# Kernel tuning notes

Hardware: AMD Instinct MI355X
Metric: run time of the kernel (lower is better)

Reference implementation:

```python
import jax, jax.numpy as jnp
import numpy as np

N = 50000      # num_labels (nodes)
HID = 64       # hidden_dim
HEADS = 4
CH = 16        # hidden_dim // 4 per head
R = 4          # relations
E = 200000     # edges per relation
DEPTH = 2
SLOPE = 0.2    # GATv2 leaky_relu negative slope
EPS = 1e-5     # LayerNorm eps


def layer_norm(x, g, b):
    mu = jnp.mean(x, axis=-1, keepdims=True)
    var = jnp.mean((x - mu) ** 2, axis=-1, keepdims=True)
    return (x - mu) / jnp.sqrt(var + EPS) * g + b


def setup_inputs() -> dict:
    key = jax.random.key(0)
    ks = jax.random.split(key, 8)
    # edges with src != dst (PyG remove_self_loops is then a no-op)
    src = jax.random.randint(ks[0], (R, E), 0, N, dtype=jnp.int32)
    off = jax.random.randint(ks[1], (R, E), 1, N, dtype=jnp.int32)
    dst = ((src + off) % N).astype(jnp.int32)
    edge_index = jnp.stack([src, dst], axis=1)  # [R, 2, E]
    s = 1.0 / np.sqrt(HID)
    return {
        "label_embeddings": jax.random.normal(ks[2], (N, HID), jnp.float32) * 0.5,
        "entry_w": jax.random.normal(ks[3], (HID, HID), jnp.float32) * s,
        "entry_b": jnp.zeros((HID,), jnp.float32),
        "entry_ln_g": jnp.ones((HID,), jnp.float32),
        "entry_ln_b": jnp.zeros((HID,), jnp.float32),
        "conv_wl": jax.random.normal(ks[4], (DEPTH, R, HID, HEADS * CH), jnp.float32) * s,
        "conv_wr": jax.random.normal(ks[5], (DEPTH, R, HID, HEADS * CH), jnp.float32) * s,
        "conv_att": jax.random.normal(ks[6], (DEPTH, R, HEADS, CH), jnp.float32) * (1.0 / np.sqrt(CH)),
        "conv_bias": jnp.zeros((DEPTH, R, HEADS * CH), jnp.float32),
        "norm_g": jnp.ones((HID,), jnp.float32),
        "norm_b": jnp.zeros((HID,), jnp.float32),
        "edge_index": edge_index,
    }


def _gatv2_layer(x, wl, wr, att, bias, src, dst):
    """One GATv2Conv over one relation. x:[N,HID]; returns [N, HEADS*CH]."""
    xl = (x @ wl).reshape(N, HEADS, CH)  # source transform
    xr = (x @ wr).reshape(N, HEADS, CH)  # target transform
    m = xl[src] + xr[dst]                          # [E+N, HEADS, CH]
    e = jnp.einsum('ehc,hc->eh', jax.nn.leaky_relu(m, SLOPE), att)  # [E+N, HEADS]
    # segment softmax over incoming edges of each dst node
    emax = jax.ops.segment_max(e, dst, num_segments=N)  # [N, HEADS]
    a = jnp.exp(e - emax[dst])
    denom = jax.ops.segment_sum(a, dst, num_segments=N)
    alpha = a / denom[dst]                          # every node has a self-loop -> denom > 0
    msg = xl[src] * alpha[..., None]                # [E+N, HEADS, CH]
    out = jax.ops.segment_sum(msg, dst, num_segments=N).reshape(N, HEADS * CH)
    return out + bias


def reference(label_embeddings, entry_w, entry_b, entry_ln_g, entry_ln_b,
              conv_wl, conv_wr, conv_att, conv_bias, norm_g, norm_b, edge_index):
    x = jax.nn.gelu(layer_norm(label_embeddings @ entry_w + entry_b, entry_ln_g, entry_ln_b),
                    approximate=False)
    loop = jnp.arange(N, dtype=edge_index.dtype)
    for layer in range(DEPTH):
        outs = []
        for r in range(R):
            src = jnp.concatenate([edge_index[r, 0], loop])  # add self-loops (PyG default)
            dst = jnp.concatenate([edge_index[r, 1], loop])
            outs.append(_gatv2_layer(x, conv_wl[layer, r], conv_wr[layer, r],
                                     conv_att[layer, r], conv_bias[layer, r], src, dst))
        x = sum(outs) / R                              # HeteroConv aggr='mean'
        x = layer_norm(jax.nn.gelu(x, approximate=False), norm_g, norm_b)  # dropout = identity (eval)
    return x
```

## Files before the change

kernel.cpp:

```cpp
#include <hip/hip_runtime.h>
#include <hip/hip_bf16.h>

#define NN 50000
#define RR 4
#define EE 200000

typedef __hip_bfloat16 bf16;
typedef __attribute__((ext_vector_type(8))) short short8;
typedef __attribute__((ext_vector_type(4))) float float4v;
typedef __attribute__((ext_vector_type(2))) float float2v;

__device__ __forceinline__ unsigned short f2bu(float v) {
    bf16 h = __float2bfloat16(v);
    return *(unsigned short*)&h;
}
__device__ __forceinline__ float ldf(const void* p, int i, int isbf) {
    return isbf ? __bfloat162float(((const bf16*)p)[i]) : ((const float*)p)[i];
}
__device__ __forceinline__ int dtype_isbf(const void* lg) {
    return ((const unsigned*)lg)[0] == 0x3F803F80u;
}
__device__ __forceinline__ float gelu_exact(float x) {
    return 0.5f * x * (1.0f + erff(x * 0.70710678118654752f));
}
__device__ __forceinline__ float2v bp2(unsigned u) {
    float2v f;
    f.x = __uint_as_float(u << 16);
    f.y = __uint_as_float(u & 0xffff0000u);
    return f;
}
__device__ __forceinline__ float2v lrelu2(float2v m) {
    float2v s = m * 0.2f;
    float2v r;
    r.x = fmaxf(m.x, s.x);
    r.y = fmaxf(m.y, s.y);
    return r;
}

#define PW_ENTRY_W 0
#define PW_ENTRY_B 4096
#define PW_LN_G    4160
#define PW_LN_B    4224
#define PW_WL      4288
#define PW_ATT     69824
#define PW_BIAS    70336
#define PW_NG      70848
#define PW_NB      70912
#define PW_TOT     70976

#define WT_ELEMS (2 * RR * 128 * 64)
#define SCAN_N (RR * NN)
#define NSB 196
#define ESB 196

__global__ __launch_bounds__(1024) void cvt_k(const void* ew, const void* eb, const void* lg,
                                              const void* lb, const void* wl, const void* wr,
                                              const void* at, const void* bi, const void* ng,
                                              const void* nb,
                                              float* __restrict__ P, bf16* __restrict__ WT,
                                              int* __restrict__ cnt) {
    int i = blockIdx.x * 1024 + threadIdx.x;
    int isbf = dtype_isbf(lg);
    if (i < SCAN_N) cnt[i] = 0;
    if (i < WT_ELEMS) {
        int k = i & 63;
        int c = (i >> 6) & 127;
        int lr = i >> 13;
        float v = (c < 64) ? ldf(wl, (lr * 64 + k) * 64 + c, isbf)
                           : ldf(wr, (lr * 64 + k) * 64 + (c - 64), isbf);
        WT[i] = __float2bfloat16(v);
    }
    if (i < PW_TOT) {
        const void* src = nullptr;
        int off = 0;
        if (i < PW_ENTRY_B)      { src = ew; off = i - PW_ENTRY_W; }
        else if (i < PW_LN_G)    { src = eb; off = i - PW_ENTRY_B; }
        else if (i < PW_LN_B)    { src = lg; off = i - PW_LN_G; }
        else if (i < PW_WL)      { src = lb; off = i - PW_LN_B; }
        else if (i < PW_ATT)     { src = nullptr; }
        else if (i < PW_BIAS)    { src = at; off = i - PW_ATT; }
        else if (i < PW_NG)      { src = bi; off = i - PW_BIAS; }
        else if (i < PW_NB)      { src = ng; off = i - PW_NG; }
        else                     { src = nb; off = i - PW_NB; }
        if (src) P[i] = ldf(src, off, isbf);
    }
}

#define HIST_BLOCKS 782
#define ENTRY_BLOCKS 2500
#define ENTRY_WAVES (ENTRY_BLOCKS * 4)
__global__ __launch_bounds__(256) void scent_k(const int* __restrict__ ei,
                                               int* __restrict__ cnt,
                                               unsigned char* __restrict__ slot8,
                                               const void* __restrict__ emb,
                                               const void* __restrict__ lg,
                                               const float* __restrict__ P,
                                               bf16* __restrict__ xout) {
    int b = blockIdx.x;
    if (b < HIST_BLOCKS) {
        int base = b * 1024 + threadIdx.x;
#pragma unroll
        for (int j = 0; j < 4; j++) {
            int idx = base + j * 256;
            if (idx < RR * EE) {
                int r = idx / EE;
                int e = idx - r * EE;
                int d = ei[r * 2 * EE + EE + e];
                int p = atomicAdd(&cnt[r * NN + d], 1);
                slot8[idx] = (unsigned char)p;
            }
        }
        return;
    }
    int wv = (b - HIST_BLOCKS) * 4 + (threadIdx.x >> 6);
    int c = threadIdx.x & 63;
    int isbf = dtype_isbf(lg);
    for (int j = 0; j < 5; j++) {
        int node = wv + j * ENTRY_WAVES;
        float ev = ldf(emb, node * 64 + c, isbf);
        float acc = 0.f;
#pragma unroll 8
        for (int k = 0; k < 64; k++) {
            float xv = __shfl(ev, k, 64);
            acc += xv * P[PW_ENTRY_W + k * 64 + c];
        }
        acc += P[PW_ENTRY_B + c];
        float s = acc;
#pragma unroll
        for (int m = 1; m < 64; m <<= 1) s += __shfl_xor(s, m, 64);
        float mu = s * (1.f / 64.f);
        float d = acc - mu;
        float vs = d * d;
#pragma unroll
        for (int m = 1; m < 64; m <<= 1) vs += __shfl_xor(vs, m, 64);
        float var = vs * (1.f / 64.f);
        float y = d * rsqrtf(var + 1e-5f) * P[PW_LN_G + c] + P[PW_LN_B + c];
        xout[node * 64 + c] = __float2bfloat16(gelu_exact(y));
    }
}

__global__ __launch_bounds__(256) void scanA_k(const int* __restrict__ cnt,
                                               int* __restrict__ bsum) {
    int b = blockIdx.x, t = threadIdx.x;
    int s = 0;
#pragma unroll
    for (int j = 0; j < 4; j++) {
        int i = b * 1024 + j * 256 + t;
        if (i < SCAN_N) s += cnt[i];
    }
#pragma unroll
    for (int m = 1; m < 64; m <<= 1) s += __shfl_xor(s, m, 64);
    __shared__ int ws[4];
    if ((t & 63) == 0) ws[t >> 6] = s;
    __syncthreads();
    if (t == 0) bsum[b] = ws[0] + ws[1] + ws[2] + ws[3];
}

__global__ void scanB_k(int* __restrict__ bsum, int* __restrict__ rp) {
    int l = threadIdx.x;
    int i0 = l * 4;
    int v0 = (i0 + 0 < NSB) ? bsum[i0 + 0] : 0;
    int v1 = (i0 + 1 < NSB) ? bsum[i0 + 1] : 0;
    int v2 = (i0 + 2 < NSB) ? bsum[i0 + 2] : 0;
    int v3 = (i0 + 3 < NSB) ? bsum[i0 + 3] : 0;
    int ts = v0 + v1 + v2 + v3;
    int inc = ts;
#pragma unroll
    for (int m = 1; m < 64; m <<= 1) {
        int y = __shfl_up(inc, m, 64);
        if (l >= m) inc += y;
    }
    int run = inc - ts;
    if (i0 + 0 < NSB) { bsum[i0 + 0] = run; run += v0; }
    if (i0 + 1 < NSB) { bsum[i0 + 1] = run; run += v1; }
    if (i0 + 2 < NSB) { bsum[i0 + 2] = run; run += v2; }
    if (i0 + 3 < NSB) { bsum[i0 + 3] = run; run += v3; }
    if (l == 63) rp[SCAN_N] = inc;
}

__global__ __launch_bounds__(256) void scanC_k(const int* __restrict__ cnt,
                                               const int* __restrict__ bsum,
                                               int* __restrict__ rp) {
    int b = blockIdx.x, t = threadIdx.x;
    int i0 = b * 1024 + t * 4;
    int v0 = (i0 + 0 < SCAN_N) ? cnt[i0 + 0] : 0;
    int v1 = (i0 + 1 < SCAN_N) ? cnt[i0 + 1] : 0;
    int v2 = (i0 + 2 < SCAN_N) ? cnt[i0 + 2] : 0;
    int v3 = (i0 + 3 < SCAN_N) ? cnt[i0 + 3] : 0;
    int ts = v0 + v1 + v2 + v3;
    int lane = t & 63, w = t >> 6;
    int inc = ts;
#pragma unroll
    for (int m = 1; m < 64; m <<= 1) {
        int y = __shfl_up(inc, m, 64);
        if (lane >= m) inc += y;
    }
    __shared__ int ws[4];
    if (lane == 63) ws[w] = inc;
    __syncthreads();
    int run = bsum[b];
    for (int k = 0; k < w; k++) run += ws[k];
    run += inc - ts;
    if (i0 + 0 < SCAN_N) { rp[i0 + 0] = run; run += v0; }
    if (i0 + 1 < SCAN_N) { rp[i0 + 1] = run; run += v1; }
    if (i0 + 2 < SCAN_N) { rp[i0 + 2] = run; run += v2; }
    if (i0 + 3 < SCAN_N) { rp[i0 + 3] = run; run += v3; }
}

#define GR 80
__global__ __launch_bounds__(256) void gemm_m(const bf16* __restrict__ X,
                                              const bf16* __restrict__ WTlayer,
                                              bf16* __restrict__ xlB,
                                              bf16* __restrict__ xrB,
                                              const int* __restrict__ ei,
                                              const unsigned char* __restrict__ slot8,
                                              const int* __restrict__ rp,
                                              unsigned short* __restrict__ col,
                                              int scatBlocks) {
    int bx = blockIdx.x;
    int r = blockIdx.y;
    if (bx < scatBlocks) {
        const int* eis = ei + r * 2 * EE;
#pragma unroll
        for (int j = 0; j < 4; j++) {
            int e = bx * 1024 + j * 256 + threadIdx.x;
            if (e < EE) {
                int s = eis[e];
                int d = eis[EE + e];
                int p = slot8[r * EE + e];
                col[rp[r * NN + d] + p] = (unsigned short)s;
            }
        }
        return;
    }
    const short* Xs = (const short*)X;
    const short* WT = (const short*)(WTlayer + (size_t)r * 8192);
    bf16* xl = xlB + (size_t)r * NN * 64;
    bf16* xr = xrB + (size_t)r * NN * 64;

    __shared__ float sh[16 * 132];
    int t = threadIdx.x;
    int w = t >> 6;
    int lane = t & 63;
    int m = lane & 15, kq = lane >> 4;
    int row0 = (bx - scatBlocks) * GR;

    short8 b0[2], b1[2];
    int c0t[2];
#pragma unroll
    for (int tile = 0; tile < 2; tile++) {
        int ct = w * 2 + tile;
        int c0 = ct * 16 + m;
        c0t[tile] = c0;
        const short* bp = WT + c0 * 64 + kq * 8;
        b0[tile] = *(const short8*)bp;
        b1[tile] = *(const short8*)(bp + 32);
    }

    const short* ap = Xs + (row0 + m) * 64 + kq * 8;
    short8 a0 = *(const short8*)ap;
    short8 a1 = *(const short8*)(ap + 32);

    for (int g = 0; g < 5; g++) {
        short8 na0, na1;
        if (g < 4) {
            const short* np = ap + (g + 1) * 16 * 64;
            na0 = *(const short8*)np;
            na1 = *(const short8*)(np + 32);
        }
#pragma unroll
        for (int tile = 0; tile < 2; tile++) {
            float4v acc = {0.f, 0.f, 0.f, 0.f};
            asm volatile(
                "v_mfma_f32_16x16x32_bf16 %0, %1, %2, %0\n\t"
                "v_mfma_f32_16x16x32_bf16 %0, %3, %4, %0\n\t"
                "s_nop 7\n\t"
                "s_nop 7"
                : "+v"(acc)
                : "v"(a0), "v"(b0[tile]), "v"(a1), "v"(b1[tile]));
#pragma unroll
            for (int i = 0; i < 4; i++) sh[(kq * 4 + i) * 132 + c0t[tile]] = acc[i];
        }
        __syncthreads();
        {
            int row = t >> 4, cg = (t & 15) * 8;
            float v0 = sh[row * 132 + cg + 0], v1 = sh[row * 132 + cg + 1];
            float v2 = sh[row * 132 + cg + 2], v3 = sh[row * 132 + cg + 3];
            float v4 = sh[row * 132 + cg + 4], v5 = sh[row * 132 + cg + 5];
            float v6 = sh[row * 132 + cg + 6], v7 = sh[row * 132 + cg + 7];
            uint4 u;
            u.x = ((unsigned)f2bu(v1) << 16) | f2bu(v0);
            u.y = ((unsigned)f2bu(v3) << 16) | f2bu(v2);
            u.z = ((unsigned)f2bu(v5) << 16) | f2bu(v4);
            u.w = ((unsigned)f2bu(v7) << 16) | f2bu(v6);
            size_t grow = row0 + g * 16 + row;
            if (cg < 64) *(uint4*)&xl[grow * 64 + cg] = u;
            else         *(uint4*)&xr[grow * 64 + (cg - 64)] = u;
        }
        __syncthreads();
        a0 = na0; a1 = na1;
    }
}

__device__ __forceinline__ void edge_accum(uint4 u0, uint4 u1, bool act,
                                           const float2v at2[8], const float2v xr2[8],
                                           float2v A2[8], float& D) {
    float2v x2[8];
    x2[0] = bp2(u0.x); x2[1] = bp2(u0.y); x2[2] = bp2(u0.z); x2[3] = bp2(u0.w);
    x2[4] = bp2(u1.x); x2[5] = bp2(u1.y); x2[6] = bp2(u1.z); x2[7] = bp2(u1.w);
    float2v t2 = (float2v){0.f, 0.f};
#pragma unroll
    for (int i = 0; i < 8; i++)
        t2 = t2 + lrelu2(x2[i] + xr2[i]) * at2[i];
    float tt = t2.x + t2.y;
    float p = act ? exp2f(tt) : 0.f;
    D += p;
    float2v p2 = (float2v){p, p};
#pragma unroll
    for (int i = 0; i < 8; i++) A2[i] = A2[i] + p2 * x2[i];
}

__global__ __launch_bounds__(256) void aggfin_k(const bf16* __restrict__ xlB,
                                                const bf16* __restrict__ xrB,
                                                const float* __restrict__ attL,
                                                const float* __restrict__ biasL,
                                                const int* __restrict__ rp,
                                                const unsigned short* __restrict__ col,
                                                const float* __restrict__ P,
                                                const void* __restrict__ lg,
                                                void* __restrict__ outp,
                                                int finalOut) {
    __shared__ float shRes[RR][4][68];
    int t = threadIdx.x;
    int r = t >> 6;
    int lane = t & 63;
    int nodeBase = blockIdx.x * 4;
    int nn = lane >> 4, es = (lane >> 2) & 3, h = lane & 3;
    int node = nodeBase + nn;

    const unsigned* xl = (const unsigned*)(xlB + (size_t)r * NN * 64);
    const unsigned* xr = (const unsigned*)(xrB + (size_t)r * NN * 64);
    const float* att = attL + r * 64;
    const float* bias = biasL + r * 64;

    int idx = r * NN + node;
    int base = rp[idx];
    int cn = rp[idx + 1] - base;
    const uint4* qr = (const uint4*)(xr + (size_t)node * 32 + h * 8);
    uint4 r0 = qr[0], r1 = qr[1];

    const unsigned short* bucket = col + base;
    int c0raw = (es > 0) ? (int)bucket[es - 1] : node;
    int c1raw = (int)bucket[es + 3];

    unsigned s0 = (unsigned)c0raw < (unsigned)NN ? (unsigned)c0raw : (unsigned)(NN - 1);
    unsigned s1 = (unsigned)c1raw < (unsigned)NN ? (unsigned)c1raw : (unsigned)(NN - 1);
    const uint4* q0 = (const uint4*)(xl + (size_t)s0 * 32 + h * 8);
    uint4 u0 = q0[0], u1 = q0[1];
    const uint4* q1 = (const uint4*)(xl + (size_t)s1 * 32 + h * 8);
    uint4 w0 = q1[0], w1 = q1[1];

    float2v at2[8], xr2[8];
    {
        const float4* apv = (const float4*)(att + h * 16);
#pragma unroll
        for (int i = 0; i < 4; i++) {
            float4 a = apv[i];
            at2[2 * i].x = a.x * 1.44269504f; at2[2 * i].y = a.y * 1.44269504f;
            at2[2 * i + 1].x = a.z * 1.44269504f; at2[2 * i + 1].y = a.w * 1.44269504f;
        }
        xr2[0] = bp2(r0.x); xr2[1] = bp2(r0.y); xr2[2] = bp2(r0.z); xr2[3] = bp2(r0.w);
        xr2[4] = bp2(r1.x); xr2[5] = bp2(r1.y); xr2[6] = bp2(r1.z); xr2[7] = bp2(r1.w);
    }
    int total = cn + 1;
    int kmax = total;
    kmax = max(kmax, __shfl_xor(kmax, 16, 64));
    kmax = max(kmax, __shfl_xor(kmax, 32, 64));

    float2v A2[8];
#pragma unroll
    for (int i = 0; i < 8; i++) A2[i] = (float2v){0.f, 0.f};
    float D = 0.f;

    edge_accum(u0, u1, es < total, at2, xr2, A2, D);
    edge_accum(w0, w1, es + 4 < total, at2, xr2, A2, D);

    for (int k = es + 8; k < kmax; k += 4) {
        bool act = k < total;
        int sr = act ? (int)bucket[k - 1] : node;
        const uint4* q = (const uint4*)(xl + (size_t)sr * 32 + h * 8);
        uint4 t0 = q[0], t1 = q[1];
        edge_accum(t0, t1, act, at2, xr2, A2, D);
    }

    D += __shfl_xor(D, 4, 64);
    D += __shfl_xor(D, 8, 64);
#pragma unroll
    for (int i = 0; i < 8; i++) {
        A2[i].x += __shfl_xor(A2[i].x, 4, 64);
        A2[i].x += __shfl_xor(A2[i].x, 8, 64);
        A2[i].y += __shfl_xor(A2[i].y, 4, 64);
        A2[i].y += __shfl_xor(A2[i].y, 8, 64);
    }
    if (es == 0) {
        float inv = __builtin_amdgcn_rcpf(D);
        const float4* bp = (const float4*)(bias + h * 16);
        float* dst = &shRes[r][nn][h * 16];
#pragma unroll
        for (int i = 0; i < 4; i++) {
            float4 b = bp[i];
            dst[4 * i + 0] = A2[2 * i].x * inv + b.x;
            dst[4 * i + 1] = A2[2 * i].y * inv + b.y;
            dst[4 * i + 2] = A2[2 * i + 1].x * inv + b.z;
            dst[4 * i + 3] = A2[2 * i + 1].y * inv + b.w;
        }
    }
    __syncthreads();
    int wn = t >> 6, c = t & 63;
    float v = shRes[0][wn][c] + shRes[1][wn][c] + shRes[2][wn][c] + shRes[3][wn][c];
    v = gelu_exact(v * 0.25f);
    float s = v;
#pragma unroll
    for (int m = 1; m < 64; m <<= 1) s += __shfl_xor(s, m, 64);
    float mu = s * (1.f / 64.f);
    float d = v - mu;
    float vs = d * d;
#pragma unroll
    for (int m = 1; m < 64; m <<= 1) vs += __shfl_xor(vs, m, 64);
    float var = vs * (1.f / 64.f);
    float y = d * rsqrtf(var + 1e-5f) * P[PW_NG + c] + P[PW_NB + c];
    size_t o = (size_t)(nodeBase + wn) * 64 + c;
    if (!finalOut) {
        ((bf16*)outp)[o] = __float2bfloat16(y);
    } else {
        if (dtype_isbf(lg)) ((bf16*)outp)[o] = __float2bfloat16(y);
        else                ((float*)outp)[o] = y;
    }
}

extern "C" void kernel_launch(void* const* d_in, const int* in_sizes, int n_in,
                              void* d_out, int out_size, void* d_ws, size_t ws_size,
                              hipStream_t stream) {
    const void* emb = d_in[0];
    const void* lg  = d_in[3];
    const int*  ei  = (const int*)d_in[11];

    const size_t BUF = (size_t)NN * 64;

    bf16* X   = (bf16*)d_ws;
    bf16* XL  = X + BUF;
    bf16* XR  = XL + RR * BUF;
    bf16* WT  = XR + RR * BUF;
    float* P  = (float*)(WT + WT_ELEMS);
    int* cnt  = (int*)(P + PW_TOT);
    int* rp   = cnt + SCAN_N;
    int* bsum = rp + SCAN_N + 1;
    unsigned short* col = (unsigned short*)(bsum + 256);
    unsigned char* slot8 = (unsigned char*)(col + RR * EE + 64);

    int cvtN = SCAN_N;
    cvt_k<<<(cvtN + 1023) / 1024, 1024, 0, stream>>>(d_in[1], d_in[2], d_in[3], d_in[4],
                                                     d_in[5], d_in[6], d_in[7], d_in[8],
                                                     d_in[9], d_in[10], P, WT, cnt);

    scent_k<<<HIST_BLOCKS + ENTRY_BLOCKS, 256, 0, stream>>>(ei, cnt, slot8, emb, lg, P, X);

    scanA_k<<<NSB, 256, 0, stream>>>(cnt, bsum);
    scanB_k<<<1, 64, 0, stream>>>(bsum, rp);
    scanC_k<<<NSB, 256, 0, stream>>>(cnt, bsum, rp);

    int gemmBlocks = 625;
    int nodeBlocks = NN / 4;

    for (int l = 0; l < 2; l++) {
        int sb = (l == 0) ? ESB : 0;
        gemm_m<<<dim3(sb + gemmBlocks, RR), 256, 0, stream>>>(
            X, WT + (size_t)l * RR * 8192, XL, XR, ei, slot8, rp, col, sb);
        aggfin_k<<<nodeBlocks, 256, 0, stream>>>(
            XL, XR, P + PW_ATT + (size_t)l * RR * 64, P + PW_BIAS + (size_t)l * RR * 64,
            rp, col, P, lg, (l == 0) ? (void*)X : d_out, l);
    }
}
```

Baseline: 323.6 us.

## Fold weight conversion into histogram kernel, overlap partial scan with first GEMM

```diff
diff --git a/kernel.cpp b/kernel.cpp
--- a/kernel.cpp
+++ b/kernel.cpp
@@ -51,54 +51,29 @@
 #define WT_ELEMS (2 * RR * 128 * 64)
 #define SCAN_N (RR * NN)
 #define NSB 196
-#define ESB 196
-
-__global__ __launch_bounds__(1024) void cvt_k(const void* ew, const void* eb, const void* lg,
-                                              const void* lb, const void* wl, const void* wr,
-                                              const void* at, const void* bi, const void* ng,
-                                              const void* nb,
-                                              float* __restrict__ P, bf16* __restrict__ WT,
-                                              int* __restrict__ cnt) {
-    int i = blockIdx.x * 1024 + threadIdx.x;
-    int isbf = dtype_isbf(lg);
-    if (i < SCAN_N) cnt[i] = 0;
-    if (i < WT_ELEMS) {
-        int k = i & 63;
-        int c = (i >> 6) & 127;
-        int lr = i >> 13;
-        float v = (c < 64) ? ldf(wl, (lr * 64 + k) * 64 + c, isbf)
-                           : ldf(wr, (lr * 64 + k) * 64 + (c - 64), isbf);
-        WT[i] = __float2bfloat16(v);
-    }
-    if (i < PW_TOT) {
-        const void* src = nullptr;
-        int off = 0;
-        if (i < PW_ENTRY_B)      { src = ew; off = i - PW_ENTRY_W; }
-        else if (i < PW_LN_G)    { src = eb; off = i - PW_ENTRY_B; }
-        else if (i < PW_LN_B)    { src = lg; off = i - PW_LN_G; }
-        else if (i < PW_WL)      { src = lb; off = i - PW_LN_B; }
-        else if (i < PW_ATT)     { src = nullptr; }
-        else if (i < PW_BIAS)    { src = at; off = i - PW_ATT; }
-        else if (i < PW_NG)      { src = bi; off = i - PW_BIAS; }
-        else if (i < PW_NB)      { src = ng; off = i - PW_NG; }
-        else                     { src = nb; off = i - PW_NB; }
-        if (src) P[i] = ldf(src, off, isbf);
-    }
-}
+#define SCANA_PB 49
 
 #define HIST_BLOCKS 782
+#define CVT_BLOCKS  196
 #define ENTRY_BLOCKS 2500
 #define ENTRY_WAVES (ENTRY_BLOCKS * 4)
-__global__ __launch_bounds__(256) void scent_k(const int* __restrict__ ei,
+__global__ __launch_bounds__(256) void mega1_k(const int* __restrict__ ei,
                                                int* __restrict__ cnt,
                                                unsigned char* __restrict__ slot8,
                                                const void* __restrict__ emb,
-                                               const void* __restrict__ lg,
-                                               const float* __restrict__ P,
+                                               const void* ew, const void* eb,
+                                               const void* lg, const void* lb,
+                                               const void* wl, const void* wr,
+                                               const void* at, const void* bi,
+                                               const void* ng, const void* nb,
+                                               float* __restrict__ P,
+                                               bf16* __restrict__ WT,
                                                bf16* __restrict__ xout) {
     int b = blockIdx.x;
+    int t = threadIdx.x;
+    int isbf = dtype_isbf(lg);
     if (b < HIST_BLOCKS) {
-        int base = b * 1024 + threadIdx.x;
+        int base = b * 1024 + t;
 #pragma unroll
         for (int j = 0; j < 4; j++) {
             int idx = base + j * 256;
@@ -112,9 +87,37 @@
         }
         return;
     }
-    int wv = (b - HIST_BLOCKS) * 4 + (threadIdx.x >> 6);
-    int c = threadIdx.x & 63;
-    int isbf = dtype_isbf(lg);
+    if (b < HIST_BLOCKS + CVT_BLOCKS) {
+#pragma unroll
+        for (int j = 0; j < 4; j++) {
+            int i = (b - HIST_BLOCKS) * 1024 + j * 256 + t;
+            if (i < WT_ELEMS) {
+                int k = i & 63;
+                int c = (i >> 6) & 127;
+                int lr = i >> 13;
+                float v = (c < 64) ? ldf(wl, (lr * 64 + k) * 64 + c, isbf)
+                                   : ldf(wr, (lr * 64 + k) * 64 + (c - 64), isbf);
+                WT[i] = __float2bfloat16(v);
+            }
+            if (i < PW_TOT) {
+                const void* src = nullptr;
+                int off = 0;
+                if (i < PW_ENTRY_B)      { src = ew; off = i - PW_ENTRY_W; }
+                else if (i < PW_LN_G)    { src = eb; off = i - PW_ENTRY_B; }
+                else if (i < PW_LN_B)    { src = lg; off = i - PW_LN_G; }
+                else if (i < PW_WL)      { src = lb; off = i - PW_LN_B; }
+                else if (i < PW_ATT)     { src = nullptr; }
+                else if (i < PW_BIAS)    { src = at; off = i - PW_ATT; }
+                else if (i < PW_NG)      { src = bi; off = i - PW_BIAS; }
+                else if (i < PW_NB)      { src = ng; off = i - PW_NG; }
+                else                     { src = nb; off = i - PW_NB; }
+                if (src) P[i] = ldf(src, off, isbf);
+            }
+        }
+        return;
+    }
+    int wv = (b - HIST_BLOCKS - CVT_BLOCKS) * 4 + (t >> 6);
+    int c = t & 63;
     for (int j = 0; j < 5; j++) {
         int node = wv + j * ENTRY_WAVES;
         float ev = ldf(emb, node * 64 + c, isbf);
@@ -122,9 +125,9 @@
 #pragma unroll 8
         for (int k = 0; k < 64; k++) {
             float xv = __shfl(ev, k, 64);
-            acc += xv * P[PW_ENTRY_W + k * 64 + c];
-        }
-        acc += P[PW_ENTRY_B + c];
+            acc += xv * ldf(ew, k * 64 + c, isbf);
+        }
+        acc += ldf(eb, c, isbf);
         float s = acc;
 #pragma unroll
         for (int m = 1; m < 64; m <<= 1) s += __shfl_xor(s, m, 64);
@@ -134,26 +137,9 @@
 #pragma unroll
         for (int m = 1; m < 64; m <<= 1) vs += __shfl_xor(vs, m, 64);
         float var = vs * (1.f / 64.f);
-        float y = d * rsqrtf(var + 1e-5f) * P[PW_LN_G + c] + P[PW_LN_B + c];
+        float y = d * rsqrtf(var + 1e-5f) * ldf(lg, c, isbf) + ldf(lb, c, isbf);
         xout[node * 64 + c] = __float2bfloat16(gelu_exact(y));
     }
-}
-
-__global__ __launch_bounds__(256) void scanA_k(const int* __restrict__ cnt,
-                                               int* __restrict__ bsum) {
-    int b = blockIdx.x, t = threadIdx.x;
-    int s = 0;
-#pragma unroll
-    for (int j = 0; j < 4; j++) {
-        int i = b * 1024 + j * 256 + t;
-        if (i < SCAN_N) s += cnt[i];
-    }
-#pragma unroll
-    for (int m = 1; m < 64; m <<= 1) s += __shfl_xor(s, m, 64);
-    __shared__ int ws[4];
-    if ((t & 63) == 0) ws[t >> 6] = s;
-    __syncthreads();
-    if (t == 0) bsum[b] = ws[0] + ws[1] + ws[2] + ws[3];
 }
 
 __global__ void scanB_k(int* __restrict__ bsum, int* __restrict__ rp) {
@@ -207,30 +193,51 @@
     if (i0 + 3 < SCAN_N) { rp[i0 + 3] = run; run += v3; }
 }
 
+__global__ __launch_bounds__(256) void scat_k(const int* __restrict__ ei,
+                                              const unsigned char* __restrict__ slot8,
+                                              const int* __restrict__ rp,
+                                              unsigned short* __restrict__ col) {
+    int bx = blockIdx.x, r = blockIdx.y;
+    const int* eis = ei + r * 2 * EE;
+#pragma unroll
+    for (int j = 0; j < 4; j++) {
+        int e = bx * 1024 + j * 256 + threadIdx.x;
+        if (e < EE) {
+            int s = eis[e];
+            int d = eis[EE + e];
+            int p = slot8[r * EE + e];
+            col[rp[r * NN + d] + p] = (unsigned short)s;
+        }
+    }
+}
+
 #define GR 80
 __global__ __launch_bounds__(256) void gemm_m(const bf16* __restrict__ X,
                                               const bf16* __restrict__ WTlayer,
                                               bf16* __restrict__ xlB,
                                               bf16* __restrict__ xrB,
-                                              const int* __restrict__ ei,
-                                              const unsigned char* __restrict__ slot8,
-                                              const int* __restrict__ rp,
-                                              unsigned short* __restrict__ col,
-                                              int scatBlocks) {
+                                              const int* __restrict__ cnt,
+                                              int* __restrict__ bsum,
+                                              int scanBlk) {
     int bx = blockIdx.x;
     int r = blockIdx.y;
-    if (bx < scatBlocks) {
-        const int* eis = ei + r * 2 * EE;
+    __shared__ float sh[16 * 132];
+    if (bx < scanBlk) {
+        int a = r * scanBlk + bx;
+        int t = threadIdx.x;
+        int s = 0;
 #pragma unroll
         for (int j = 0; j < 4; j++) {
-            int e = bx * 1024 + j * 256 + threadIdx.x;
-            if (e < EE) {
-                int s = eis[e];
-                int d = eis[EE + e];
-                int p = slot8[r * EE + e];
-                col[rp[r * NN + d] + p] = (unsigned short)s;
-            }
-        }
+            int i = a * 1024 + j * 256 + t;
+            if (i < SCAN_N) s += cnt[i];
+        }
+#pragma unroll
+        for (int m = 1; m < 64; m <<= 1) s += __shfl_xor(s, m, 64);
+        if ((t & 63) == 0) sh[t >> 6] = __int_as_float(s);
+        __syncthreads();
+        if (t == 0)
+            bsum[a] = __float_as_int(sh[0]) + __float_as_int(sh[1]) +
+                      __float_as_int(sh[2]) + __float_as_int(sh[3]);
         return;
     }
     const short* Xs = (const short*)X;
@@ -238,12 +245,11 @@
     bf16* xl = xlB + (size_t)r * NN * 64;
     bf16* xr = xrB + (size_t)r * NN * 64;
 
-    __shared__ float sh[16 * 132];
     int t = threadIdx.x;
     int w = t >> 6;
     int lane = t & 63;
     int m = lane & 15, kq = lane >> 4;
-    int row0 = (bx - scatBlocks) * GR;
+    int row0 = (bx - scanBlk) * GR;
 
     short8 b0[2], b1[2];
     int c0t[2];
@@ -458,26 +464,25 @@
     unsigned short* col = (unsigned short*)(bsum + 256);
     unsigned char* slot8 = (unsigned char*)(col + RR * EE + 64);
 
-    int cvtN = SCAN_N;
-    cvt_k<<<(cvtN + 1023) / 1024, 1024, 0, stream>>>(d_in[1], d_in[2], d_in[3], d_in[4],
-                                                     d_in[5], d_in[6], d_in[7], d_in[8],
-                                                     d_in[9], d_in[10], P, WT, cnt);
-
-    scent_k<<<HIST_BLOCKS + ENTRY_BLOCKS, 256, 0, stream>>>(ei, cnt, slot8, emb, lg, P, X);
-
-    scanA_k<<<NSB, 256, 0, stream>>>(cnt, bsum);
+    hipMemsetAsync(cnt, 0, SCAN_N * sizeof(int), stream);
+
+    mega1_k<<<HIST_BLOCKS + CVT_BLOCKS + ENTRY_BLOCKS, 256, 0, stream>>>(
+        ei, cnt, slot8, emb, d_in[1], d_in[2], d_in[3], d_in[4], d_in[5], d_in[6],
+        d_in[7], d_in[8], d_in[9], d_in[10], P, WT, X);
+
+    int nodeBlocks = NN / 4;
+
+    gemm_m<<<dim3(SCANA_PB + 625, RR), 256, 0, stream>>>(
+        X, WT, XL, XR, cnt, bsum, SCANA_PB);
     scanB_k<<<1, 64, 0, stream>>>(bsum, rp);
     scanC_k<<<NSB, 256, 0, stream>>>(cnt, bsum, rp);
-
-    int gemmBlocks = 625;
-    int nodeBlocks = NN / 4;
-
-    for (int l = 0; l < 2; l++) {
-        int sb = (l == 0) ? ESB : 0;
-        gemm_m<<<dim3(sb + gemmBlocks, RR), 256, 0, stream>>>(
-            X, WT + (size_t)l * RR * 8192, XL, XR, ei, slot8, rp, col, sb);
-        aggfin_k<<<nodeBlocks, 256, 0, stream>>>(
-            XL, XR, P + PW_ATT + (size_t)l * RR * 64, P + PW_BIAS + (size_t)l * RR * 64,
-            rp, col, P, lg, (l == 0) ? (void*)X : d_out, l);
-    }
-}
+    scat_k<<<dim3(196, RR), 256, 0, stream>>>(ei, slot8, rp, col);
+
+    aggfin_k<<<nodeBlocks, 256, 0, stream>>>(
+        XL, XR, P + PW_ATT, P + PW_BIAS, rp, col, P, lg, (void*)X, 0);
+
+    gemm_m<<<dim3(625, RR), 256, 0, stream>>>(
+        X, WT + (size_t)RR * 8192, XL, XR, cnt, bsum, 0);
+    aggfin_k<<<nodeBlocks, 256, 0, stream>>>(
+        XL, XR, P + PW_ATT + RR * 64, P + PW_BIAS + RR * 64, rp, col, P, lg, d_out, 1);
+}
```

New measurement: 335.1 us. 3.6% more time.
